# Performance work log

Measured on AMD Instinct MI355X. Metric: run time of the kernel, lower is better.

The kernel has to match this reference:

```python
import jax, jax.numpy as jnp
import numpy as np

N = 50000
E = 800000
D_IN = 384
D_H = 128
D_MLP = 128
K = 16


def layer_norm(x, g, b, eps=1e-5):
    m = x.mean(-1, keepdims=True)
    v = ((x - m) ** 2).mean(-1, keepdims=True)
    return (x - m) / jnp.sqrt(v + eps) * g + b


def setup_inputs() -> dict:
    key = jax.random.key(0)
    ks = jax.random.split(key, 16)
    s = lambda d: 1.0 / np.sqrt(d)
    return {
        "x": jax.random.normal(ks[0], (N, D_IN), jnp.float32),
        "edge_index": jax.random.randint(ks[1], (2, E), 0, N, jnp.int64),
        # GCNConv 1
        "W1": jax.random.normal(ks[2], (D_IN, D_H), jnp.float32) * s(D_IN),
        "b1": jnp.zeros((D_H,), jnp.float32),
        "g1": jnp.ones((D_H,), jnp.float32),
        "be1": jnp.zeros((D_H,), jnp.float32),
        # GCNConv 2
        "W2": jax.random.normal(ks[3], (D_H, D_H), jnp.float32) * s(D_H),
        "b2": jnp.zeros((D_H,), jnp.float32),
        "g2": jnp.ones((D_H,), jnp.float32),
        "be2": jnp.zeros((D_H,), jnp.float32),
        # residual projection (input_dim != conv_hidden)
        "rW": jax.random.normal(ks[4], (D_IN, D_H), jnp.float32) * s(D_IN),
        "rb": jnp.zeros((D_H,), jnp.float32),
        "rg": jnp.ones((D_H,), jnp.float32),
        "rbe": jnp.zeros((D_H,), jnp.float32),
        # MLP head
        "mW1": jax.random.normal(ks[5], (D_H, D_MLP), jnp.float32) * s(D_H),
        "mb1": jnp.zeros((D_MLP,), jnp.float32),
        "mg": jnp.ones((D_MLP,), jnp.float32),
        "mbe": jnp.zeros((D_MLP,), jnp.float32),
        "mW2": jax.random.normal(ks[6], (D_MLP, K), jnp.float32) * s(D_MLP),
        "mb2": jnp.zeros((K,), jnp.float32),
    }


def reference(x, edge_index, W1, b1, g1, be1, W2, b2, g2, be2,
              rW, rb, rg, rbe, mW1, mb1, mg, mbe, mW2, mb2):
    n = x.shape[0]
    loops = jnp.arange(n, dtype=edge_index.dtype)
    src = jnp.concatenate([edge_index[0], loops])  # [E+N]
    dst = jnp.concatenate([edge_index[1], loops])
    # symmetric GCN normalization with self-loops
    deg = jax.ops.segment_sum(jnp.ones_like(src, x.dtype), dst, num_segments=n)
    dinv = jnp.where(deg > 0, jax.lax.rsqrt(deg), 0.0)
    norm = dinv[src] * dinv[dst]  # [E+N]

    def gcn_conv(h, W, b):
        hw = h @ W  # [N, D_H]
        msg = hw[src] * norm[:, None]  # gather + scale, [E+N, D_H]
        return jax.ops.segment_sum(msg, dst, num_segments=n) + b

    # layer 1 with projected residual
    h = jax.nn.elu(layer_norm(gcn_conv(x, W1, b1), g1, be1))
    h = h + layer_norm(x @ rW + rb, rg, rbe)
    # layer 2 with identity residual
    h = jax.nn.elu(layer_norm(gcn_conv(h, W2, b2), g2, be2)) + h
    # MLP head (dropout inactive in eval) + softmax over clusters
    z = jax.nn.elu(layer_norm(h @ mW1 + mb1, mg, mbe))
    H = z @ mW2 + mb2
    return jax.nn.softmax(H, axis=1)
```

## Files before the change

kernel.cpp:

```cpp
#include <hip/hip_runtime.h>

#define DH 128

typedef __attribute__((ext_vector_type(8))) short short8;
typedef __attribute__((ext_vector_type(4))) float f32x4;

__device__ __forceinline__ float wave_sum(float v) {
    #pragma unroll
    for (int o = 32; o > 0; o >>= 1) v += __shfl_xor(v, o, 64);
    return v;
}

__device__ __forceinline__ void ln_pair(float v0, float v1, float& o0, float& o1) {
    float m = wave_sum(v0 + v1) * (1.f / 128.f);
    float d0 = v0 - m, d1 = v1 - m;
    float var = wave_sum(d0 * d0 + d1 * d1) * (1.f / 128.f);
    float inv = rsqrtf(var + 1e-5f);
    o0 = d0 * inv; o1 = d1 * inv;
}

__device__ __forceinline__ float elu(float x) { return x > 0.f ? x : expm1f(x); }

__device__ __forceinline__ unsigned short f2bf(float f) {
    unsigned u = __float_as_uint(f);
    u += 0x7fffu + ((u >> 16) & 1u);
    return (unsigned short)(u >> 16);
}
__device__ __forceinline__ float bfl(unsigned u) { return __uint_as_float(u << 16); }
__device__ __forceinline__ float bfh(unsigned u) { return __uint_as_float(u & 0xffff0000u); }
__device__ __forceinline__ unsigned pack_bf2(float a, float b) {
    return (unsigned)f2bf(a) | ((unsigned)f2bf(b) << 16);
}
__device__ __forceinline__ short8 cvt8(float4 v0, float4 v1) {
    short8 o;
    o[0] = (short)f2bf(v0.x); o[1] = (short)f2bf(v0.y);
    o[2] = (short)f2bf(v0.z); o[3] = (short)f2bf(v0.w);
    o[4] = (short)f2bf(v1.x); o[5] = (short)f2bf(v1.y);
    o[6] = (short)f2bf(v1.z); o[7] = (short)f2bf(v1.w);
    return o;
}

__global__ void deg_count_k(const int* __restrict__ dst, int* __restrict__ deg, int E) {
    int e = blockIdx.x * 256 + threadIdx.x;
    if (e < E) atomicAdd(&deg[dst[e]], 1);
}

__global__ __launch_bounds__(1024) void scan_part_k(const int* __restrict__ deg,
                                                    int* __restrict__ rowptr,
                                                    int* __restrict__ bsum,
                                                    float* __restrict__ dinv, int n)
{
    __shared__ int wsum[16];
    const int tid = threadIdx.x, lane = tid & 63, wid = tid >> 6;
    int i = blockIdx.x * 1024 + tid;
    int v = (i < n) ? deg[i] : 0;
    if (i < n) dinv[i] = rsqrtf((float)(v + 1));
    int s = v;
    #pragma unroll
    for (int o = 1; o < 64; o <<= 1) {
        int t = __shfl_up(s, o, 64);
        if (lane >= o) s += t;
    }
    if (lane == 63) wsum[wid] = s;
    __syncthreads();
    if (tid < 16) {
        int ws = wsum[tid];
        #pragma unroll
        for (int o = 1; o < 16; o <<= 1) {
            int t = __shfl_up(ws, o, 64);
            if (tid >= o) ws += t;
        }
        wsum[tid] = ws;
    }
    __syncthreads();
    int excl = (wid ? wsum[wid - 1] : 0) + s - v;
    if (i < n) rowptr[i] = excl;
    if (tid == 0) bsum[blockIdx.x] = wsum[15];
}

__global__ void scan_top_k(int* __restrict__ bsum, int* __restrict__ rowptr_n, int nb) {
    int lane = threadIdx.x;
    int carry = 0;
    for (int base = 0; base < nb; base += 64) {
        int i = base + lane;
        int v = (i < nb) ? bsum[i] : 0;
        int s = v;
        #pragma unroll
        for (int o = 1; o < 64; o <<= 1) {
            int t = __shfl_up(s, o, 64);
            if (lane >= o) s += t;
        }
        if (i < nb) bsum[i] = carry + s - v;
        carry += __shfl(s, 63, 64);
    }
    if (lane == 0) *rowptr_n = carry;
}

__global__ void scan_add_k(const int* __restrict__ bsum, int* __restrict__ rowptr,
                           int* __restrict__ cursor, int n)
{
    int i = blockIdx.x * 256 + threadIdx.x;
    if (i < n) {
        int v = rowptr[i] + bsum[i >> 10];
        rowptr[i] = v;
        cursor[i] = v;
    }
}

__global__ void fill_k(const int* __restrict__ src, const int* __restrict__ dst,
                       const float* __restrict__ dinv, int* __restrict__ cursor,
                       int2* __restrict__ csr, int E)
{
    int e = blockIdx.x * 256 + threadIdx.x;
    if (e < E) {
        int s = src[e], d = dst[e];
        float w = dinv[s] * dinv[d];
        int p = atomicAdd(&cursor[d], 1);
        csr[p] = make_int2(s, __float_as_int(w));
    }
}

__global__ void repack_zero_k(const float* __restrict__ W1, const float* __restrict__ rW,
                              const float* __restrict__ W2, const float* __restrict__ mW1,
                              unsigned short* __restrict__ Wp, int* __restrict__ deg, int n)
{
    int idx = blockIdx.x * 256 + threadIdx.x;
    if (idx < n) deg[idx] = 0;
    if (idx >= 131072) return;
    const float* W; int base;
    if (idx < 49152)       { W = W1;  base = 0; }
    else if (idx < 98304)  { W = rW;  base = 49152; }
    else if (idx < 114688) { W = W2;  base = 98304; }
    else                   { W = mW1; base = 114688; }
    int l = idx - base;
    int kb = l >> 12, rem = l & 4095;
    int nn = rem >> 5, ki = rem & 31;
    Wp[idx] = f2bf(W[(kb * 32 + ki) * DH + nn]);
}

template<int K, int NV, bool AF32>
__global__ __launch_bounds__(256, 4) void mfma_gemm(
    const void* __restrict__ Avoid,
    const unsigned short* __restrict__ Bp1, const float* __restrict__ ba,
    const unsigned short* __restrict__ Bp2, const float* __restrict__ bb,
    unsigned short* __restrict__ outa, unsigned short* __restrict__ outb, int n)
{
    constexpr int NKB = K / 32;
    __shared__ __align__(16) unsigned short smem[12288];

    const int tid = threadIdx.x;
    const int wid = tid >> 6, lane = tid & 63;
    const int m16 = lane & 15, q = lane >> 4;

    const int nwg = gridDim.x;
    const int qc = nwg >> 3, rc = nwg & 7;
    const int xcd = blockIdx.x & 7, ix = blockIdx.x >> 3;
    const int work = (xcd < rc ? xcd * (qc + 1) : rc * (qc + 1) + (xcd - rc) * qc) + ix;
    const int rblk = work / NV;
    const int var  = work - rblk * NV;

    const int mat = (NV == 4) ? (var >> 1) : 0;
    const int c0  = (NV == 4) ? ((var & 1) * 64) : (var * 64);
    const unsigned short* Bp = mat ? Bp2 : Bp1;
    unsigned short* outp = mat ? outb : outa;
    const float* bias = mat ? bb : ba;
    const long long rowbase = (long long)rblk * 128;

    unsigned short* smA = smem;
    unsigned short* smB = smem + 8192;

    const int aq0 = tid >> 7,        ar0 = tid & 127;
    const int aq1 = (tid + 256) >> 7, ar1 = tid & 127;
    long long gr0 = rowbase + ar0; if (gr0 > (long long)n - 1) gr0 = n - 1;
    long long gr1 = rowbase + ar1; if (gr1 > (long long)n - 1) gr1 = n - 1;
    const int qb = tid >> 6, clb = tid & 63;

    const float* Af = (const float*)Avoid;
    const unsigned short* Ah = (const unsigned short*)Avoid;
    const float* pAf0 = AF32 ? Af + gr0 * K + aq0 * 8 : nullptr;
    const float* pAf1 = AF32 ? Af + gr1 * K + aq1 * 8 : nullptr;
    const unsigned short* pAh0 = AF32 ? nullptr : Ah + gr0 * K + aq0 * 8;
    const unsigned short* pAh1 = AF32 ? nullptr : Ah + gr1 * K + aq1 * 8;
    const unsigned short* pB = Bp + (c0 + clb) * 32 + qb * 8;

    unsigned short* dA0 = smA + aq0 * 1024 + ar0 * 8;
    unsigned short* dA1 = smA + aq1 * 1024 + ar1 * 8;
    unsigned short* dB  = smB + qb * 512 + clb * 8;

    float4 raf[2][2][2];
    short8 rah[2][2];
    short8 rbv[2];

    auto loadT = [&](int kb, int buf) {
        if constexpr (AF32) {
            raf[buf][0][0] = *(const float4*)(pAf0 + kb * 32);
            raf[buf][0][1] = *(const float4*)(pAf0 + kb * 32 + 4);
            raf[buf][1][0] = *(const float4*)(pAf1 + kb * 32);
            raf[buf][1][1] = *(const float4*)(pAf1 + kb * 32 + 4);
        } else {
            rah[buf][0] = *(const short8*)(pAh0 + kb * 32);
            rah[buf][1] = *(const short8*)(pAh1 + kb * 32);
        }
        rbv[buf] = *(const short8*)(pB + kb * 4096);
    };
    auto writeT = [&](int buf) {
        if constexpr (AF32) {
            *(short8*)(dA0 + buf * 4096) = cvt8(raf[buf][0][0], raf[buf][0][1]);
            *(short8*)(dA1 + buf * 4096) = cvt8(raf[buf][1][0], raf[buf][1][1]);
        } else {
            *(short8*)(dA0 + buf * 4096) = rah[buf][0];
            *(short8*)(dA1 + buf * 4096) = rah[buf][1];
        }
        *(short8*)(dB + buf * 2048) = rbv[buf];
    };

    f32x4 acc[2][4];
    const f32x4 zero = {0.f, 0.f, 0.f, 0.f};
    #pragma unroll
    for (int mi = 0; mi < 2; ++mi)
        #pragma unroll
        for (int nj = 0; nj < 4; ++nj) acc[mi][nj] = zero;

    const unsigned short* fa_base = smA + q * 1024 + (wid * 32 + m16) * 8;
    const unsigned short* fb_base = smB + q * 512 + m16 * 8;

    loadT(0, 0);
    if constexpr (NKB > 1) loadT(1, 1);
    writeT(0);
    __syncthreads();

    #pragma unroll
    for (int kb = 0; kb < NKB; ++kb) {
        const int buf = kb & 1;
        short8 af0 = *(const short8*)(fa_base + buf * 4096);
        short8 af1 = *(const short8*)(fa_base + buf * 4096 + 128);
        short8 bf[4];
        #pragma unroll
        for (int nj = 0; nj < 4; ++nj)
            bf[nj] = *(const short8*)(fb_base + buf * 2048 + nj * 128);
        if (kb + 2 < NKB) loadT(kb + 2, kb & 1);
        if (kb + 1 < NKB) writeT((kb + 1) & 1);
        #pragma unroll
        for (int nj = 0; nj < 4; ++nj) {
            acc[0][nj] = __builtin_amdgcn_mfma_f32_16x16x32_bf16(af0, bf[nj], acc[0][nj], 0, 0, 0);
            acc[1][nj] = __builtin_amdgcn_mfma_f32_16x16x32_bf16(af1, bf[nj], acc[1][nj], 0, 0, 0);
        }
        __syncthreads();
    }

    #pragma unroll
    for (int nj = 0; nj < 4; ++nj) {
        int cl = nj * 16 + m16;
        float bv = bias ? bias[c0 + cl] : 0.f;
        #pragma unroll
        for (int mi = 0; mi < 2; ++mi)
            #pragma unroll
            for (int r = 0; r < 4; ++r)
                smem[(wid * 32 + mi * 16 + q * 4 + r) * 72 + cl] = f2bf(acc[mi][nj][r] + bv);
    }
    __syncthreads();
    #pragma unroll
    for (int h = 0; h < 4; ++h) {
        int idx = tid + h * 256;
        int row = idx >> 3, c8 = idx & 7;
        long long grow = rowbase + row;
        if (grow < n)
            *(short8*)(outp + grow * DH + c0 + c8 * 8) = *(const short8*)(smem + row * 72 + c8 * 8);
    }
}

__device__ __forceinline__ void gather_row(
    const unsigned* __restrict__ hw, const int2* __restrict__ csr,
    int beg, int end, int lane, float& o0, float& o1)
{
    float a0 = 0.f, a1 = 0.f, b0 = 0.f, b1 = 0.f;
    float c0 = 0.f, c1 = 0.f, d0 = 0.f, d1 = 0.f;
    int p = beg;
    for (; p + 7 < end; p += 8) {
        int2 e0 = csr[p],     e1 = csr[p + 1], e2 = csr[p + 2], e3 = csr[p + 3];
        int2 e4 = csr[p + 4], e5 = csr[p + 5], e6 = csr[p + 6], e7 = csr[p + 7];
        unsigned u0 = hw[(long long)e0.x * 64 + lane];
        unsigned u1 = hw[(long long)e1.x * 64 + lane];
        unsigned u2 = hw[(long long)e2.x * 64 + lane];
        unsigned u3 = hw[(long long)e3.x * 64 + lane];
        unsigned u4 = hw[(long long)e4.x * 64 + lane];
        unsigned u5 = hw[(long long)e5.x * 64 + lane];
        unsigned u6 = hw[(long long)e6.x * 64 + lane];
        unsigned u7 = hw[(long long)e7.x * 64 + lane];
        float w0 = __int_as_float(e0.y), w1 = __int_as_float(e1.y);
        float w2 = __int_as_float(e2.y), w3 = __int_as_float(e3.y);
        float w4 = __int_as_float(e4.y), w5 = __int_as_float(e5.y);
        float w6 = __int_as_float(e6.y), w7 = __int_as_float(e7.y);
        a0 = fmaf(w0, bfl(u0), a0);  a1 = fmaf(w0, bfh(u0), a1);
        b0 = fmaf(w1, bfl(u1), b0);  b1 = fmaf(w1, bfh(u1), b1);
        c0 = fmaf(w2, bfl(u2), c0);  c1 = fmaf(w2, bfh(u2), c1);
        d0 = fmaf(w3, bfl(u3), d0);  d1 = fmaf(w3, bfh(u3), d1);
        a0 = fmaf(w4, bfl(u4), a0);  a1 = fmaf(w4, bfh(u4), a1);
        b0 = fmaf(w5, bfl(u5), b0);  b1 = fmaf(w5, bfh(u5), b1);
        c0 = fmaf(w6, bfl(u6), c0);  c1 = fmaf(w6, bfh(u6), c1);
        d0 = fmaf(w7, bfl(u7), d0);  d1 = fmaf(w7, bfh(u7), d1);
    }
    for (; p + 3 < end; p += 4) {
        int2 e0 = csr[p], e1 = csr[p + 1], e2 = csr[p + 2], e3 = csr[p + 3];
        unsigned u0 = hw[(long long)e0.x * 64 + lane];
        unsigned u1 = hw[(long long)e1.x * 64 + lane];
        unsigned u2 = hw[(long long)e2.x * 64 + lane];
        unsigned u3 = hw[(long long)e3.x * 64 + lane];
        float w0 = __int_as_float(e0.y), w1 = __int_as_float(e1.y);
        float w2 = __int_as_float(e2.y), w3 = __int_as_float(e3.y);
        a0 = fmaf(w0, bfl(u0), a0);  a1 = fmaf(w0, bfh(u0), a1);
        b0 = fmaf(w1, bfl(u1), b0);  b1 = fmaf(w1, bfh(u1), b1);
        c0 = fmaf(w2, bfl(u2), c0);  c1 = fmaf(w2, bfh(u2), c1);
        d0 = fmaf(w3, bfl(u3), d0);  d1 = fmaf(w3, bfh(u3), d1);
    }
    for (; p < end; ++p) {
        int2 e0 = csr[p];
        unsigned u0 = hw[(long long)e0.x * 64 + lane];
        float w0 = __int_as_float(e0.y);
        a0 = fmaf(w0, bfl(u0), a0);
        a1 = fmaf(w0, bfh(u0), a1);
    }
    o0 = (a0 + b0) + (c0 + d0);
    o1 = (a1 + b1) + (c1 + d1);
}

__global__ __launch_bounds__(256) void gfuse1_k(
    const unsigned* __restrict__ hw, const unsigned* __restrict__ proj,
    const int* __restrict__ rowptr, const int2* __restrict__ csr,
    const float* __restrict__ dinv,
    const float* __restrict__ b1, const float* __restrict__ g1, const float* __restrict__ be1,
    const float* __restrict__ rg, const float* __restrict__ rbe,
    unsigned* __restrict__ hout, int n)
{
    int row = blockIdx.x * 4 + (threadIdx.x >> 6);
    if (row >= n) return;
    int lane = threadIdx.x & 63;
    float a0, a1;
    gather_row(hw, csr, rowptr[row], rowptr[row + 1], lane, a0, a1);
    long long off = (long long)row * 64;
    float di = dinv[row], sl = di * di;
    unsigned us = hw[off + lane];
    float2 bv  = *(const float2*)(b1 + 2 * lane);
    float2 gv  = *(const float2*)(g1 + 2 * lane);
    float2 bev = *(const float2*)(be1 + 2 * lane);
    float2 rgv = *(const float2*)(rg + 2 * lane);
    float2 rbv = *(const float2*)(rbe + 2 * lane);
    float v0 = a0 + sl * bfl(us) + bv.x;
    float v1 = a1 + sl * bfh(us) + bv.y;
    float o0, o1; ln_pair(v0, v1, o0, o1);
    float t0 = elu(o0 * gv.x + bev.x);
    float t1 = elu(o1 * gv.y + bev.y);
    unsigned up = proj[off + lane];
    float q0, q1; ln_pair(bfl(up), bfh(up), q0, q1);
    hout[off + lane] = pack_bf2(t0 + q0 * rgv.x + rbv.x, t1 + q1 * rgv.y + rbv.y);
}

__global__ __launch_bounds__(256) void gfuse2_k(
    const unsigned* __restrict__ hw, const unsigned* __restrict__ hprev,
    const int* __restrict__ rowptr, const int2* __restrict__ csr,
    const float* __restrict__ dinv,
    const float* __restrict__ b2, const float* __restrict__ g2, const float* __restrict__ be2,
    unsigned* __restrict__ h2, int n)
{
    int row = blockIdx.x * 4 + (threadIdx.x >> 6);
    if (row >= n) return;
    int lane = threadIdx.x & 63;
    float a0, a1;
    gather_row(hw, csr, rowptr[row], rowptr[row + 1], lane, a0, a1);
    long long off = (long long)row * 64;
    float di = dinv[row], sl = di * di;
    unsigned us = hw[off + lane];
    float2 bv  = *(const float2*)(b2 + 2 * lane);
    float2 gv  = *(const float2*)(g2 + 2 * lane);
    float2 bev = *(const float2*)(be2 + 2 * lane);
    float v0 = a0 + sl * bfl(us) + bv.x;
    float v1 = a1 + sl * bfh(us) + bv.y;
    float o0, o1; ln_pair(v0, v1, o0, o1);
    float t0 = elu(o0 * gv.x + bev.x);
    float t1 = elu(o1 * gv.y + bev.y);
    unsigned uh = hprev[off + lane];
    h2[off + lane] = pack_bf2(t0 + bfl(uh), t1 + bfh(uh));
}

__global__ __launch_bounds__(256) void head_k(
    const unsigned* __restrict__ zraw, const float* __restrict__ g, const float* __restrict__ be,
    const float* __restrict__ mW2, const float* __restrict__ mb2,
    float* __restrict__ out, int n)
{
    int row = blockIdx.x * 4 + (threadIdx.x >> 6);
    if (row >= n) return;
    int lane = threadIdx.x & 63;
    unsigned u = zraw[(long long)row * 64 + lane];
    float o0, o1; ln_pair(bfl(u), bfh(u), o0, o1);
    float2 gv  = *(const float2*)(g + 2 * lane);
    float2 bev = *(const float2*)(be + 2 * lane);
    float z0 = elu(o0 * gv.x + bev.x);
    float z1 = elu(o1 * gv.y + bev.y);
    int k = lane & 15, seg = lane >> 4;
    float acc = 0.f;
    #pragma unroll
    for (int t = 0; t < 16; ++t) {
        int srcl = seg * 16 + t;
        float zz0 = __shfl(z0, srcl, 64);
        float zz1 = __shfl(z1, srcl, 64);
        int c = seg * 32 + 2 * t;
        acc = fmaf(zz0, mW2[c * 16 + k], acc);
        acc = fmaf(zz1, mW2[(c + 1) * 16 + k], acc);
    }
    acc += __shfl_xor(acc, 32, 64);
    acc += __shfl_xor(acc, 16, 64);
    float hk = acc + mb2[k];
    float mx = hk;
    #pragma unroll
    for (int o = 8; o > 0; o >>= 1) mx = fmaxf(mx, __shfl_xor(mx, o, 64));
    float e = expf(hk - mx);
    float s = e;
    #pragma unroll
    for (int o = 8; o > 0; o >>= 1) s += __shfl_xor(s, o, 64);
    if (lane < 16) out[(long long)row * 16 + k] = e / s;
}

static inline size_t align16(size_t x) { return (x + 15) & ~(size_t)15; }

extern "C" void kernel_launch(void* const* d_in, const int* in_sizes, int n_in,
                              void* d_out, int out_size, void* d_ws, size_t ws_size,
                              hipStream_t stream)
{
    const float* x   = (const float*)d_in[0];
    const int*   ei  = (const int*)d_in[1];
    const float* W1  = (const float*)d_in[2];
    const float* b1  = (const float*)d_in[3];
    const float* g1  = (const float*)d_in[4];
    const float* be1 = (const float*)d_in[5];
    const float* W2  = (const float*)d_in[6];
    const float* b2  = (const float*)d_in[7];
    const float* g2  = (const float*)d_in[8];
    const float* be2 = (const float*)d_in[9];
    const float* rW  = (const float*)d_in[10];
    const float* rb  = (const float*)d_in[11];
    const float* rg  = (const float*)d_in[12];
    const float* rbe = (const float*)d_in[13];
    const float* mW1 = (const float*)d_in[14];
    const float* mb1 = (const float*)d_in[15];
    const float* mg  = (const float*)d_in[16];
    const float* mbe = (const float*)d_in[17];
    const float* mW2 = (const float*)d_in[18];
    const float* mb2 = (const float*)d_in[19];
    float* out = (float*)d_out;

    const int n = in_sizes[0] / 384;
    const int E = in_sizes[1] / 2;
    const int* src = ei;
    const int* dst = ei + E;

    char* w = (char*)d_ws;
    int* deg     = (int*)w;   w += align16((size_t)n * 4);
    int* rowptr  = (int*)w;   w += align16((size_t)(n + 1) * 4);
    int* cursor  = (int*)w;   w += align16((size_t)n * 4);
    float* dinv  = (float*)w; w += align16((size_t)n * 4);
    int* bsum    = (int*)w;   w += align16((size_t)1024 * 4);
    int2* csr    = (int2*)w;  w += align16((size_t)E * 8);
    unsigned short* hw1  = (unsigned short*)w; w += align16((size_t)n * DH * 2);
    unsigned short* proj = (unsigned short*)w; w += align16((size_t)n * DH * 2);
    unsigned short* hbuf = (unsigned short*)w; w += align16((size_t)n * DH * 2);
    unsigned short* Wp   = (unsigned short*)w; w += align16((size_t)131072 * 2);
    unsigned short* Wp1 = Wp;
    unsigned short* Wpr = Wp + 49152;
    unsigned short* Wp2 = Wp + 98304;
    unsigned short* WpM = Wp + 114688;
    unsigned short* hw2  = hw1;
    unsigned short* h2   = proj;
    unsigned short* zraw = hbuf;

    int gE = (E + 255) / 256;
    int gN = (n + 255) / 256;
    int nb = (n + 1023) / 1024;
    int rblks = (n + 127) / 128;
    int gRow4 = (n + 3) / 4;

    repack_zero_k<<<512, 256, 0, stream>>>(W1, rW, W2, mW1, Wp, deg, n);

    deg_count_k<<<gE, 256, 0, stream>>>(dst, deg, E);
    scan_part_k<<<nb, 1024, 0, stream>>>(deg, rowptr, bsum, dinv, n);
    scan_top_k<<<1, 64, 0, stream>>>(bsum, rowptr + n, nb);
    scan_add_k<<<gN, 256, 0, stream>>>(bsum, rowptr, cursor, n);
    fill_k<<<gE, 256, 0, stream>>>(src, dst, dinv, cursor, csr, E);

    mfma_gemm<384, 4, true><<<rblks * 4, 256, 0, stream>>>(x, Wp1, nullptr, Wpr, rb, hw1, proj, n);
    gfuse1_k<<<gRow4, 256, 0, stream>>>((unsigned*)hw1, (unsigned*)proj, rowptr, csr, dinv,
                                        b1, g1, be1, rg, rbe, (unsigned*)hbuf, n);

    mfma_gemm<128, 2, false><<<rblks * 2, 256, 0, stream>>>(hbuf, Wp2, nullptr, nullptr, nullptr, hw2, nullptr, n);
    gfuse2_k<<<gRow4, 256, 0, stream>>>((unsigned*)hw2, (unsigned*)hbuf, rowptr, csr, dinv,
                                        b2, g2, be2, (unsigned*)h2, n);

    mfma_gemm<128, 2, false><<<rblks * 2, 256, 0, stream>>>(h2, WpM, mb1, nullptr, nullptr, zraw, nullptr, n);
    head_k<<<gRow4, 256, 0, stream>>>((unsigned*)zraw, mg, mbe, mW2, mb2, out, n);
}
```

Baseline: 430.9 us.

## Split GEMM into specialized kernels with coalesced row loads and XOR-swizzled LDS

Replaces the templated MFMA GEMM with two specialized kernels. The K=384 kernel now loads A rows contiguously, with four threads per row, and stores them into LDS using an XOR swizzle. This is meant to improve global coalescing and avoid LDS bank conflicts. The K=128 kernel stages the entire A tile and B slice in LDS once and then runs all four k-steps without per-step syncs, using more shared memory and lower occupancy (launch bounds 3) in exchange.

Measured after the change: 408.6 us. 5.2% less time.

```diff
diff --git a/kernel.cpp b/kernel.cpp
--- a/kernel.cpp
+++ b/kernel.cpp
@@ -38,6 +38,12 @@
     o[4] = (short)f2bf(v1.x); o[5] = (short)f2bf(v1.y);
     o[6] = (short)f2bf(v1.z); o[7] = (short)f2bf(v1.w);
     return o;
+}
+
+__device__ __forceinline__ int xcd_work(int bid, int nwg) {
+    int qc = nwg >> 3, rc = nwg & 7;
+    int xcd = bid & 7, ix = bid >> 3;
+    return (xcd < rc ? xcd * (qc + 1) : rc * (qc + 1) + (xcd - rc) * qc) + ix;
 }
 
 __global__ void deg_count_k(const int* __restrict__ dst, int* __restrict__ deg, int E) {
@@ -138,79 +144,54 @@
     Wp[idx] = f2bf(W[(kb * 32 + ki) * DH + nn]);
 }
 
-template<int K, int NV, bool AF32>
-__global__ __launch_bounds__(256, 4) void mfma_gemm(
-    const void* __restrict__ Avoid,
-    const unsigned short* __restrict__ Bp1, const float* __restrict__ ba,
-    const unsigned short* __restrict__ Bp2, const float* __restrict__ bb,
+__global__ __launch_bounds__(256, 4) void gemm1_k(
+    const float* __restrict__ Af,
+    const unsigned short* __restrict__ Bp1, const unsigned short* __restrict__ Bp2,
+    const float* __restrict__ bb,
     unsigned short* __restrict__ outa, unsigned short* __restrict__ outb, int n)
 {
-    constexpr int NKB = K / 32;
+    constexpr int K = 384, NKB = 12;
     __shared__ __align__(16) unsigned short smem[12288];
+    unsigned short* smB = smem + 8192;
 
     const int tid = threadIdx.x;
     const int wid = tid >> 6, lane = tid & 63;
     const int m16 = lane & 15, q = lane >> 4;
 
-    const int nwg = gridDim.x;
-    const int qc = nwg >> 3, rc = nwg & 7;
-    const int xcd = blockIdx.x & 7, ix = blockIdx.x >> 3;
-    const int work = (xcd < rc ? xcd * (qc + 1) : rc * (qc + 1) + (xcd - rc) * qc) + ix;
-    const int rblk = work / NV;
-    const int var  = work - rblk * NV;
-
-    const int mat = (NV == 4) ? (var >> 1) : 0;
-    const int c0  = (NV == 4) ? ((var & 1) * 64) : (var * 64);
+    const int work = xcd_work(blockIdx.x, gridDim.x);
+    const int rblk = work >> 2;
+    const int var  = work & 3;
+    const int mat = var >> 1;
+    const int c0  = (var & 1) * 64;
     const unsigned short* Bp = mat ? Bp2 : Bp1;
     unsigned short* outp = mat ? outb : outa;
-    const float* bias = mat ? bb : ba;
+    const float* bias = mat ? bb : nullptr;
     const long long rowbase = (long long)rblk * 128;
 
-    unsigned short* smA = smem;
-    unsigned short* smB = smem + 8192;
-
-    const int aq0 = tid >> 7,        ar0 = tid & 127;
-    const int aq1 = (tid + 256) >> 7, ar1 = tid & 127;
-    long long gr0 = rowbase + ar0; if (gr0 > (long long)n - 1) gr0 = n - 1;
-    long long gr1 = rowbase + ar1; if (gr1 > (long long)n - 1) gr1 = n - 1;
-    const int qb = tid >> 6, clb = tid & 63;
-
-    const float* Af = (const float*)Avoid;
-    const unsigned short* Ah = (const unsigned short*)Avoid;
-    const float* pAf0 = AF32 ? Af + gr0 * K + aq0 * 8 : nullptr;
-    const float* pAf1 = AF32 ? Af + gr1 * K + aq1 * 8 : nullptr;
-    const unsigned short* pAh0 = AF32 ? nullptr : Ah + gr0 * K + aq0 * 8;
-    const unsigned short* pAh1 = AF32 ? nullptr : Ah + gr1 * K + aq1 * 8;
-    const unsigned short* pB = Bp + (c0 + clb) * 32 + qb * 8;
-
-    unsigned short* dA0 = smA + aq0 * 1024 + ar0 * 8;
-    unsigned short* dA1 = smA + aq1 * 1024 + ar1 * 8;
-    unsigned short* dB  = smB + qb * 512 + clb * 8;
+    const int row_s0 = tid >> 2, c16_0 = tid & 3;
+    const int row_s1 = (tid + 256) >> 2;
+    long long gr0 = rowbase + row_s0; if (gr0 > (long long)n - 1) gr0 = n - 1;
+    long long gr1 = rowbase + row_s1; if (gr1 > (long long)n - 1) gr1 = n - 1;
+    const float* pA0 = Af + gr0 * K + c16_0 * 8;
+    const float* pA1 = Af + gr1 * K + c16_0 * 8;
+    unsigned short* dA0 = smem + row_s0 * 32 + ((c16_0 ^ (row_s0 & 3)) * 8);
+    unsigned short* dA1 = smem + row_s1 * 32 + ((c16_0 ^ (row_s1 & 3)) * 8);
+    const unsigned short* pB = Bp + c0 * 32 + tid * 8;
+    unsigned short* dB = smB + (tid & 3) * 512 + (tid >> 2) * 8;
 
     float4 raf[2][2][2];
-    short8 rah[2][2];
     short8 rbv[2];
 
     auto loadT = [&](int kb, int buf) {
-        if constexpr (AF32) {
-            raf[buf][0][0] = *(const float4*)(pAf0 + kb * 32);
-            raf[buf][0][1] = *(const float4*)(pAf0 + kb * 32 + 4);
-            raf[buf][1][0] = *(const float4*)(pAf1 + kb * 32);
-            raf[buf][1][1] = *(const float4*)(pAf1 + kb * 32 + 4);
-        } else {
-            rah[buf][0] = *(const short8*)(pAh0 + kb * 32);
-            rah[buf][1] = *(const short8*)(pAh1 + kb * 32);
-        }
+        raf[buf][0][0] = *(const float4*)(pA0 + kb * 32);
+        raf[buf][0][1] = *(const float4*)(pA0 + kb * 32 + 4);
+        raf[buf][1][0] = *(const float4*)(pA1 + kb * 32);
+        raf[buf][1][1] = *(const float4*)(pA1 + kb * 32 + 4);
         rbv[buf] = *(const short8*)(pB + kb * 4096);
     };
     auto writeT = [&](int buf) {
-        if constexpr (AF32) {
-            *(short8*)(dA0 + buf * 4096) = cvt8(raf[buf][0][0], raf[buf][0][1]);
-            *(short8*)(dA1 + buf * 4096) = cvt8(raf[buf][1][0], raf[buf][1][1]);
-        } else {
-            *(short8*)(dA0 + buf * 4096) = rah[buf][0];
-            *(short8*)(dA1 + buf * 4096) = rah[buf][1];
-        }
+        *(short8*)(dA0 + buf * 4096) = cvt8(raf[buf][0][0], raf[buf][0][1]);
+        *(short8*)(dA1 + buf * 4096) = cvt8(raf[buf][1][0], raf[buf][1][1]);
         *(short8*)(dB + buf * 2048) = rbv[buf];
     };
 
@@ -221,11 +202,12 @@
         #pragma unroll
         for (int nj = 0; nj < 4; ++nj) acc[mi][nj] = zero;
 
-    const unsigned short* fa_base = smA + q * 1024 + (wid * 32 + m16) * 8;
+    const int frow = wid * 32 + m16;
+    const unsigned short* fa_base = smem + frow * 32 + ((q ^ (m16 & 3)) * 8);
     const unsigned short* fb_base = smB + q * 512 + m16 * 8;
 
     loadT(0, 0);
-    if constexpr (NKB > 1) loadT(1, 1);
+    loadT(1, 1);
     writeT(0);
     __syncthreads();
 
@@ -233,7 +215,7 @@
     for (int kb = 0; kb < NKB; ++kb) {
         const int buf = kb & 1;
         short8 af0 = *(const short8*)(fa_base + buf * 4096);
-        short8 af1 = *(const short8*)(fa_base + buf * 4096 + 128);
+        short8 af1 = *(const short8*)(fa_base + buf * 4096 + 512);
         short8 bf[4];
         #pragma unroll
         for (int nj = 0; nj < 4; ++nj)
@@ -248,6 +230,83 @@
         __syncthreads();
     }
 
+    #pragma unroll
+    for (int nj = 0; nj < 4; ++nj) {
+        int cl = nj * 16 + m16;
+        float bv = bias ? bias[c0 + cl] : 0.f;
+        #pragma unroll
+        for (int mi = 0; mi < 2; ++mi)
+            #pragma unroll
+            for (int r = 0; r < 4; ++r)
+                smem[(wid * 32 + mi * 16 + q * 4 + r) * 72 + cl] = f2bf(acc[mi][nj][r] + bv);
+    }
+    __syncthreads();
+    #pragma unroll
+    for (int h = 0; h < 4; ++h) {
+        int idx = tid + h * 256;
+        int row = idx >> 3, c8 = idx & 7;
+        long long grow = rowbase + row;
+        if (grow < n)
+            *(short8*)(outp + grow * DH + c0 + c8 * 8) = *(const short8*)(smem + row * 72 + c8 * 8);
+    }
+}
+
+__global__ __launch_bounds__(256, 3) void gemm_k128(
+    const unsigned short* __restrict__ A,
+    const unsigned short* __restrict__ Bp, const float* __restrict__ bias,
+    unsigned short* __restrict__ outp, int n)
+{
+    __shared__ __align__(16) unsigned short smem[24576];
+    unsigned short* smB = smem + 16384;
+
+    const int tid = threadIdx.x;
+    const int wid = tid >> 6, lane = tid & 63;
+    const int m16 = lane & 15, q = lane >> 4;
+
+    const int work = xcd_work(blockIdx.x, gridDim.x);
+    const int rblk = work >> 1;
+    const int c0 = (work & 1) * 64;
+    const long long rowbase = (long long)rblk * 128;
+
+    #pragma unroll
+    for (int r = 0; r < 8; ++r) {
+        int j = r * 256 + tid;
+        int row = j >> 4, c16 = j & 15;
+        long long grow = rowbase + row; if (grow > (long long)n - 1) grow = n - 1;
+        *(short8*)(smem + row * 128 + ((c16 ^ (row & 15)) * 8)) =
+            *(const short8*)(A + grow * 128 + c16 * 8);
+    }
+    #pragma unroll
+    for (int r = 0; r < 4; ++r) {
+        int j = r * 256 + tid;
+        int kb = j >> 8, rem = j & 255;
+        int cl = rem >> 2, qq = rem & 3;
+        *(short8*)(smB + kb * 2048 + qq * 512 + cl * 8) =
+            *(const short8*)(Bp + kb * 4096 + c0 * 32 + rem * 8);
+    }
+    __syncthreads();
+
+    f32x4 acc[2][4];
+    const f32x4 zero = {0.f, 0.f, 0.f, 0.f};
+    #pragma unroll
+    for (int mi = 0; mi < 2; ++mi)
+        #pragma unroll
+        for (int nj = 0; nj < 4; ++nj) acc[mi][nj] = zero;
+
+    const int frow = wid * 32 + m16;
+    #pragma unroll
+    for (int kb = 0; kb < 4; ++kb) {
+        short8 af0 = *(const short8*)(smem + frow * 128 + (((kb * 4 + q) ^ m16) * 8));
+        short8 af1 = *(const short8*)(smem + (frow + 16) * 128 + (((kb * 4 + q) ^ m16) * 8));
+        #pragma unroll
+        for (int nj = 0; nj < 4; ++nj) {
+            short8 bf = *(const short8*)(smB + kb * 2048 + q * 512 + (nj * 16 + m16) * 8);
+            acc[0][nj] = __builtin_amdgcn_mfma_f32_16x16x32_bf16(af0, bf, acc[0][nj], 0, 0, 0);
+            acc[1][nj] = __builtin_amdgcn_mfma_f32_16x16x32_bf16(af1, bf, acc[1][nj], 0, 0, 0);
+        }
+    }
+
+    __syncthreads();
     #pragma unroll
     for (int nj = 0; nj < 4; ++nj) {
         int cl = nj * 16 + m16;
@@ -486,14 +545,14 @@
     scan_add_k<<<gN, 256, 0, stream>>>(bsum, rowptr, cursor, n);
     fill_k<<<gE, 256, 0, stream>>>(src, dst, dinv, cursor, csr, E);
 
-    mfma_gemm<384, 4, true><<<rblks * 4, 256, 0, stream>>>(x, Wp1, nullptr, Wpr, rb, hw1, proj, n);
+    gemm1_k<<<rblks * 4, 256, 0, stream>>>(x, Wp1, Wpr, rb, hw1, proj, n);
     gfuse1_k<<<gRow4, 256, 0, stream>>>((unsigned*)hw1, (unsigned*)proj, rowptr, csr, dinv,
                                         b1, g1, be1, rg, rbe, (unsigned*)hbuf, n);
 
-    mfma_gemm<128, 2, false><<<rblks * 2, 256, 0, stream>>>(hbuf, Wp2, nullptr, nullptr, nullptr, hw2, nullptr, n);
+    gemm_k128<<<rblks * 2, 256, 0, stream>>>(hbuf, Wp2, nullptr, hw2, n);
     gfuse2_k<<<gRow4, 256, 0, stream>>>((unsigned*)hw2, (unsigned*)hbuf, rowptr, csr, dinv,
                                         b2, g2, be2, (unsigned*)h2, n);
 
-    mfma_gemm<128, 2, false><<<rblks * 2, 256, 0, stream>>>(h2, WpM, mb1, nullptr, nullptr, zraw, nullptr, n);
+    gemm_k128<<<rblks * 2, 256, 0, stream>>>(h2, WpM, mb1, zraw, n);
     head_k<<<gRow4, 256, 0, stream>>>((unsigned*)zraw, mg, mbe, mW2, mb2, out, n);
 }
```
